# Kernel tuning notes

Hardware: AMD Instinct MI355X
Metric: run time of the kernel (lower is better)

The kernel has to match this reference:

```python
import jax, jax.numpy as jnp
import numpy as np

B, V = 256, 2048
PD, MD, H = 1024, 512, 512

def setup_inputs() -> dict:
    key = jax.random.key(0)
    k1, k2, k3, k4, k5 = jax.random.split(key, 5)
    patient_emb = jax.random.normal(k1, (B, PD), dtype=jnp.float32)
    atc4_emb = jax.random.normal(k2, (V, MD), dtype=jnp.float32)
    # Linear(PD+MD -> H): weight (H, PD+MD), bias (H,)
    W1 = jax.random.normal(k3, (H, PD + MD), dtype=jnp.float32) * 0.02
    b1 = jnp.zeros((H,), dtype=jnp.float32)
    # Linear(H -> 1): weight (1, H) -> store as (H,), bias scalar
    w2 = jax.random.normal(k4, (H,), dtype=jnp.float32) * 0.05
    b2 = jnp.zeros((), dtype=jnp.float32)
    return {"patient_emb": patient_emb, "atc4_emb": atc4_emb,
            "W1": W1, "b1": b1, "w2": w2, "b2": b2}

def reference(patient_emb, atc4_emb, W1, b1, w2, b2):
    # Algebraically equivalent to cat([patient, mol]) @ W1.T:
    # split W1 into patient and mol blocks, matmul each, broadcast-add.
    W1p = W1[:, :PD]   # (H, PD)
    W1m = W1[:, PD:]   # (H, MD)
    hp = jnp.einsum('bp,hp->bh', patient_emb, W1p)   # (B, H)
    hm = jnp.einsum('vm,hm->vh', atc4_emb, W1m)      # (V, H)
    h = jnp.tanh(hp[:, None, :] + hm[None, :, :] + b1)  # (B, V, H)
    scores = jnp.einsum('bvh,h->bv', h, w2) + b2     # (B, V)
    return scores
```

## Files before the change

### kernel.cpp

```cpp
#include <hip/hip_runtime.h>
#include <hip/hip_bf16.h>
#include <math.h>

typedef __attribute__((ext_vector_type(8))) short short8;
typedef __attribute__((ext_vector_type(4))) float float4v;
typedef __attribute__((ext_vector_type(2))) float float2v;

__device__ __forceinline__ float2v lo2(float4v v) {
    return __builtin_shufflevector(v, v, 0, 1);
}
__device__ __forceinline__ float2v hi2(float4v v) {
    return __builtin_shufflevector(v, v, 2, 3);
}

__device__ __forceinline__ int2 cvt2bf16x4(float4v v) {
    union { __hip_bfloat162 h2; int i; } u0, u1;
    u0.h2 = __float22bfloat162_rn(make_float2(v.x, v.y));
    u1.h2 = __float22bfloat162_rn(make_float2(v.z, v.w));
    return make_int2(u0.i, u1.i);
}

__global__ __launch_bounds__(256) void gemm_exp(
    const float* __restrict__ patient, const float* __restrict__ atc4,
    const float* __restrict__ W1, const float* __restrict__ b1,
    float* __restrict__ EA, float* __restrict__ EM)
{
    const float* A; const float* W; const float* bias; float* T;
    int lda, K, M;
    if (blockIdx.z == 0) {
        if (blockIdx.x >= 4) return;
        A = patient; lda = 1024; K = 1024; M = 256; bias = b1; T = EA; W = W1;
    } else {
        A = atc4;    lda = 512;  K = 512;  M = 2048; bias = nullptr; T = EM; W = W1 + 1024;
    }
    const int ldw = 1536;

    __shared__ short As[64][72];
    __shared__ short Bs[64][72];
    const int t = threadIdx.x;
    const int m0 = blockIdx.x * 64;
    const int n0 = blockIdx.y * 64;
    const int wave = t >> 6;
    const int lane = t & 63;
    const int wm = (wave & 1) * 32;
    const int wn = (wave >> 1) * 32;
    const int lrow = lane & 15;
    const int quad = lane >> 4;

    float4v acc[2][2];
    #pragma unroll
    for (int i = 0; i < 2; i++)
        #pragma unroll
        for (int j = 0; j < 2; j++)
            acc[i][j] = (float4v){0.f, 0.f, 0.f, 0.f};

    const int sr = t >> 2;
    const int sc = (t & 3) * 16;

    float4v av[4], wv[4];
    {
        const float* ap = A + (size_t)(m0 + sr) * lda + sc;
        const float* wp = W + (size_t)(n0 + sr) * ldw + sc;
        #pragma unroll
        for (int ii = 0; ii < 4; ii++) {
            av[ii] = *(const float4v*)(ap + ii * 4);
            wv[ii] = *(const float4v*)(wp + ii * 4);
        }
    }

    for (int k0 = 0; k0 < K; k0 += 64) {
        #pragma unroll
        for (int ii = 0; ii < 4; ii++) {
            *(int2*)&As[sr][sc + ii * 4] = cvt2bf16x4(av[ii]);
            *(int2*)&Bs[sr][sc + ii * 4] = cvt2bf16x4(wv[ii]);
        }
        __syncthreads();
        if (k0 + 64 < K) {
            const float* ap = A + (size_t)(m0 + sr) * lda + (k0 + 64 + sc);
            const float* wp = W + (size_t)(n0 + sr) * ldw + (k0 + 64 + sc);
            #pragma unroll
            for (int ii = 0; ii < 4; ii++) {
                av[ii] = *(const float4v*)(ap + ii * 4);
                wv[ii] = *(const float4v*)(wp + ii * 4);
            }
        }
        #pragma unroll
        for (int kk = 0; kk < 64; kk += 32) {
            short8 af[2], bfr[2];
            #pragma unroll
            for (int i = 0; i < 2; i++)
                af[i] = *(const short8*)&As[wm + i * 16 + lrow][kk + quad * 8];
            #pragma unroll
            for (int j = 0; j < 2; j++)
                bfr[j] = *(const short8*)&Bs[wn + j * 16 + lrow][kk + quad * 8];
            #pragma unroll
            for (int i = 0; i < 2; i++)
                #pragma unroll
                for (int j = 0; j < 2; j++)
                    acc[i][j] = __builtin_amdgcn_mfma_f32_16x16x32_bf16(
                        af[i], bfr[j], acc[i][j], 0, 0, 0);
        }
        __syncthreads();
    }

    #pragma unroll
    for (int i = 0; i < 2; i++) {
        #pragma unroll
        for (int j = 0; j < 2; j++) {
            const int n  = n0 + wn + j * 16 + lrow;
            const int mb = m0 + wm + i * 16 + quad * 4;
            const float bn = bias ? bias[n] : 0.0f;
            float4v ev;
            #pragma unroll
            for (int r = 0; r < 4; r++)
                ev[r] = __expf(2.0f * (acc[i][j][r] + bn));
            *(float4v*)&T[(size_t)n * M + mb] = ev;
        }
    }
}

__device__ __forceinline__ void rat4(
    float2v em0, float2v em1, float2v em2, float2v em3,
    float2v a0, float2v a1, float2v a2, float2v a3,
    float2v c0, float2v c1, float2v c2, float2v c3,
    float2v& acc)
{
    const float2v one2 = {1.f, 1.f};
    float2v d0 = __builtin_elementwise_fma(em0, a0, one2);
    float2v d1 = __builtin_elementwise_fma(em1, a1, one2);
    float2v d2 = __builtin_elementwise_fma(em2, a2, one2);
    float2v d3 = __builtin_elementwise_fma(em3, a3, one2);
    float2v e01 = d0 * d1;
    float2v e23 = d2 * d3;
    float2v n01 = __builtin_elementwise_fma(d1, c0, d0 * c1);
    float2v n23 = __builtin_elementwise_fma(d3, c2, d2 * c3);
    float2v num = __builtin_elementwise_fma(n01, e23, n23 * e01);
    float2v den = e01 * e23;
    float2v r = { __builtin_amdgcn_rcpf(den.x), __builtin_amdgcn_rcpf(den.y) };
    acc = __builtin_elementwise_fma(num, r, acc);
}

__global__ __launch_bounds__(256) void pair_kernel(
    const float* __restrict__ EA, const float* __restrict__ EM,
    const float* __restrict__ w2, float* __restrict__ partial)
{
    __shared__ float sEA[32][68];
    __shared__ float sEM[32][132];
    __shared__ float4v sC4[32];
    const int t  = threadIdx.x;
    const int v0 = blockIdx.x * 128;
    const int b0 = blockIdx.y * 64;
    const int h0 = blockIdx.z * 128;
    const int tx = t & 15;
    const int ty = t >> 4;

    if (t < 32) {
        float4v wvq = *(const float4v*)(w2 + h0 + 4 * t);
        sC4[t] = -2.0f * wvq;
    }

    float2v accAL[4], accAH[4], accBL[4], accBH[4];
    #pragma unroll
    for (int i = 0; i < 4; i++) {
        accAL[i] = (float2v){0.f, 0.f};  accAH[i] = (float2v){0.f, 0.f};
        accBL[i] = (float2v){0.f, 0.f};  accBH[i] = (float2v){0.f, 0.f};
    }

    const int rS = t >> 3;
    const int cA = (t & 7) * 8;
    const int cM = (t & 7) * 16;

    float4v pA0, pA1, pM0, pM1, pM2, pM3;
    {
        const float* pa = EA + (size_t)(h0 + rS) * 256 + b0 + cA;
        pA0 = *(const float4v*)pa;  pA1 = *(const float4v*)(pa + 4);
        const float* pm = EM + (size_t)(h0 + rS) * 2048 + v0 + cM;
        pM0 = *(const float4v*)pm;       pM1 = *(const float4v*)(pm + 4);
        pM2 = *(const float4v*)(pm + 8); pM3 = *(const float4v*)(pm + 12);
    }
    *(float4v*)&sEA[rS][cA] = pA0;      *(float4v*)&sEA[rS][cA + 4] = pA1;
    *(float4v*)&sEM[rS][cM] = pM0;      *(float4v*)&sEM[rS][cM + 4] = pM1;
    *(float4v*)&sEM[rS][cM + 8] = pM2;  *(float4v*)&sEM[rS][cM + 12] = pM3;
    __syncthreads();

    #pragma unroll 1
    for (int s = 0; s < 4; s++) {
        if (s < 3) {
            const int hr = h0 + (s + 1) * 32 + rS;
            const float* pa = EA + (size_t)hr * 256 + b0 + cA;
            pA0 = *(const float4v*)pa;  pA1 = *(const float4v*)(pa + 4);
            const float* pm = EM + (size_t)hr * 2048 + v0 + cM;
            pM0 = *(const float4v*)pm;       pM1 = *(const float4v*)(pm + 4);
            pM2 = *(const float4v*)(pm + 8); pM3 = *(const float4v*)(pm + 12);
        }
        #pragma unroll 2
        for (int q = 0; q < 8; q++) {
            const int hq = 4 * q;
            const float4v ea0 = *(const float4v*)&sEA[hq    ][ty * 4];
            const float4v ea1 = *(const float4v*)&sEA[hq + 1][ty * 4];
            const float4v ea2 = *(const float4v*)&sEA[hq + 2][ty * 4];
            const float4v ea3 = *(const float4v*)&sEA[hq + 3][ty * 4];
            const float4v c = sC4[s * 8 + q];
            const float2v c0 = { c.x, c.x };
            const float2v c1 = { c.y, c.y };
            const float2v c2 = { c.z, c.z };
            const float2v c3 = { c.w, c.w };
            {
                const float4v em0 = *(const float4v*)&sEM[hq    ][tx * 4];
                const float4v em1 = *(const float4v*)&sEM[hq + 1][tx * 4];
                const float4v em2 = *(const float4v*)&sEM[hq + 2][tx * 4];
                const float4v em3 = *(const float4v*)&sEM[hq + 3][tx * 4];
                const float2v em0L = lo2(em0), em0H = hi2(em0);
                const float2v em1L = lo2(em1), em1H = hi2(em1);
                const float2v em2L = lo2(em2), em2H = hi2(em2);
                const float2v em3L = lo2(em3), em3H = hi2(em3);
                #pragma unroll
                for (int i = 0; i < 4; i++) {
                    const float2v a0 = { ea0[i], ea0[i] };
                    const float2v a1 = { ea1[i], ea1[i] };
                    const float2v a2 = { ea2[i], ea2[i] };
                    const float2v a3 = { ea3[i], ea3[i] };
                    rat4(em0L, em1L, em2L, em3L, a0, a1, a2, a3,
                         c0, c1, c2, c3, accAL[i]);
                    rat4(em0H, em1H, em2H, em3H, a0, a1, a2, a3,
                         c0, c1, c2, c3, accAH[i]);
                }
            }
            {
                const float4v em0 = *(const float4v*)&sEM[hq    ][64 + tx * 4];
                const float4v em1 = *(const float4v*)&sEM[hq + 1][64 + tx * 4];
                const float4v em2 = *(const float4v*)&sEM[hq + 2][64 + tx * 4];
                const float4v em3 = *(const float4v*)&sEM[hq + 3][64 + tx * 4];
                const float2v em0L = lo2(em0), em0H = hi2(em0);
                const float2v em1L = lo2(em1), em1H = hi2(em1);
                const float2v em2L = lo2(em2), em2H = hi2(em2);
                const float2v em3L = lo2(em3), em3H = hi2(em3);
                #pragma unroll
                for (int i = 0; i < 4; i++) {
                    const float2v a0 = { ea0[i], ea0[i] };
                    const float2v a1 = { ea1[i], ea1[i] };
                    const float2v a2 = { ea2[i], ea2[i] };
                    const float2v a3 = { ea3[i], ea3[i] };
                    rat4(em0L, em1L, em2L, em3L, a0, a1, a2, a3,
                         c0, c1, c2, c3, accBL[i]);
                    rat4(em0H, em1H, em2H, em3H, a0, a1, a2, a3,
                         c0, c1, c2, c3, accBH[i]);
                }
            }
        }
        if (s < 3) {
            __syncthreads();
            *(float4v*)&sEA[rS][cA] = pA0;      *(float4v*)&sEA[rS][cA + 4] = pA1;
            *(float4v*)&sEM[rS][cM] = pM0;      *(float4v*)&sEM[rS][cM + 4] = pM1;
            *(float4v*)&sEM[rS][cM + 8] = pM2;  *(float4v*)&sEM[rS][cM + 12] = pM3;
            __syncthreads();
        }
    }

    float4v w2q = sC4[0];
    #pragma unroll
    for (int k = 1; k < 32; k++) w2q += sC4[k];
    const float w2s = -0.5f * (w2q.x + w2q.y + w2q.z + w2q.w);

    const size_t pb = (size_t)blockIdx.z * (256 * 2048);
    #pragma unroll
    for (int i = 0; i < 4; i++) {
        const size_t row = pb + (size_t)(b0 + ty * 4 + i) * 2048 + v0 + tx * 4;
        float4v oA = { accAL[i].x + w2s, accAL[i].y + w2s,
                       accAH[i].x + w2s, accAH[i].y + w2s };
        float4v oB = { accBL[i].x + w2s, accBL[i].y + w2s,
                       accBH[i].x + w2s, accBH[i].y + w2s };
        *(float4v*)&partial[row] = oA;
        *(float4v*)&partial[row + 64] = oB;
    }
}

__global__ __launch_bounds__(256) void reduce_kernel(
    const float* __restrict__ partial, const float* __restrict__ b2,
    float* __restrict__ out)
{
    const int i = (blockIdx.x * 256 + threadIdx.x) * 4;
    const float bb = b2[0];
    float4v s = *(const float4v*)&partial[i];
    #pragma unroll
    for (int z = 1; z < 4; z++)
        s += *(const float4v*)&partial[(size_t)z * 524288 + i];
    float4v o = s + bb;
    *(float4v*)&out[i] = o;
}

extern "C" void kernel_launch(void* const* d_in, const int* in_sizes, int n_in,
                              void* d_out, int out_size, void* d_ws, size_t ws_size,
                              hipStream_t stream)
{
    const float* patient = (const float*)d_in[0];
    const float* atc4    = (const float*)d_in[1];
    const float* W1      = (const float*)d_in[2];
    const float* b1      = (const float*)d_in[3];
    const float* w2      = (const float*)d_in[4];
    const float* b2      = (const float*)d_in[5];
    float* out = (float*)d_out;
    float* ws  = (float*)d_ws;

    float* EA      = ws;
    float* EM      = ws + 131072;
    float* partial = ws + 1179648;

    gemm_exp<<<dim3(32, 8, 2), 256, 0, stream>>>(patient, atc4, W1, b1, EA, EM);
    pair_kernel<<<dim3(16, 4, 4), 256, 0, stream>>>(EA, EM, w2, partial);
    reduce_kernel<<<512, 256, 0, stream>>>(partial, b2, out);
}
```

Measured before the change: 117.3 us.

## Double-buffer pair-kernel LDS tiles and fuse split-H reduction via last-block atomics

The shared-memory tiles in the pair kernel are double-buffered, and global loads are issued two stages ahead, so each stage needs one barrier instead of two. The separate reduce kernel is removed. Each output tile's last-finishing H-split block, found through an atomic counter zeroed by the GEMM kernel, sums the four partials and adds b2. This saves a kernel launch and overlaps the reduction with other blocks, at the cost of more LDS per block, thread fences, and a serialized tail in the final blocks.

```diff
diff --git a/kernel.cpp b/kernel.cpp
--- a/kernel.cpp
+++ b/kernel.cpp
@@ -23,8 +23,11 @@
 __global__ __launch_bounds__(256) void gemm_exp(
     const float* __restrict__ patient, const float* __restrict__ atc4,
     const float* __restrict__ W1, const float* __restrict__ b1,
-    float* __restrict__ EA, float* __restrict__ EM)
+    float* __restrict__ EA, float* __restrict__ EM, int* __restrict__ ctr)
 {
+    if (blockIdx.z == 0 && blockIdx.x == 0 && blockIdx.y == 0 && threadIdx.x < 64)
+        ctr[threadIdx.x] = 0;
+
     const float* A; const float* W; const float* bias; float* T;
     int lda, K, M;
     if (blockIdx.z == 0) {
@@ -142,11 +145,14 @@
 
 __global__ __launch_bounds__(256) void pair_kernel(
     const float* __restrict__ EA, const float* __restrict__ EM,
-    const float* __restrict__ w2, float* __restrict__ partial)
+    const float* __restrict__ w2, const float* __restrict__ b2,
+    float* __restrict__ partial, float* __restrict__ out,
+    int* __restrict__ ctr)
 {
-    __shared__ float sEA[32][68];
-    __shared__ float sEM[32][132];
+    __shared__ float sEA[2][32][68];
+    __shared__ float sEM[2][32][132];
     __shared__ float4v sC4[32];
+    __shared__ int isLast;
     const int t  = threadIdx.x;
     const int v0 = blockIdx.x * 128;
     const int b0 = blockIdx.y * 64;
@@ -178,15 +184,28 @@
         pM0 = *(const float4v*)pm;       pM1 = *(const float4v*)(pm + 4);
         pM2 = *(const float4v*)(pm + 8); pM3 = *(const float4v*)(pm + 12);
     }
-    *(float4v*)&sEA[rS][cA] = pA0;      *(float4v*)&sEA[rS][cA + 4] = pA1;
-    *(float4v*)&sEM[rS][cM] = pM0;      *(float4v*)&sEM[rS][cM + 4] = pM1;
-    *(float4v*)&sEM[rS][cM + 8] = pM2;  *(float4v*)&sEM[rS][cM + 12] = pM3;
+    *(float4v*)&sEA[0][rS][cA] = pA0;      *(float4v*)&sEA[0][rS][cA + 4] = pA1;
+    *(float4v*)&sEM[0][rS][cM] = pM0;      *(float4v*)&sEM[0][rS][cM + 4] = pM1;
+    *(float4v*)&sEM[0][rS][cM + 8] = pM2;  *(float4v*)&sEM[0][rS][cM + 12] = pM3;
+    {
+        const float* pa = EA + (size_t)(h0 + 32 + rS) * 256 + b0 + cA;
+        pA0 = *(const float4v*)pa;  pA1 = *(const float4v*)(pa + 4);
+        const float* pm = EM + (size_t)(h0 + 32 + rS) * 2048 + v0 + cM;
+        pM0 = *(const float4v*)pm;       pM1 = *(const float4v*)(pm + 4);
+        pM2 = *(const float4v*)(pm + 8); pM3 = *(const float4v*)(pm + 12);
+    }
     __syncthreads();
 
     #pragma unroll 1
     for (int s = 0; s < 4; s++) {
+        const int cur = s & 1, nxt = cur ^ 1;
         if (s < 3) {
-            const int hr = h0 + (s + 1) * 32 + rS;
+            *(float4v*)&sEA[nxt][rS][cA] = pA0;      *(float4v*)&sEA[nxt][rS][cA + 4] = pA1;
+            *(float4v*)&sEM[nxt][rS][cM] = pM0;      *(float4v*)&sEM[nxt][rS][cM + 4] = pM1;
+            *(float4v*)&sEM[nxt][rS][cM + 8] = pM2;  *(float4v*)&sEM[nxt][rS][cM + 12] = pM3;
+        }
+        if (s < 2) {
+            const int hr = h0 + (s + 2) * 32 + rS;
             const float* pa = EA + (size_t)hr * 256 + b0 + cA;
             pA0 = *(const float4v*)pa;  pA1 = *(const float4v*)(pa + 4);
             const float* pm = EM + (size_t)hr * 2048 + v0 + cM;
@@ -196,20 +215,20 @@
         #pragma unroll 2
         for (int q = 0; q < 8; q++) {
             const int hq = 4 * q;
-            const float4v ea0 = *(const float4v*)&sEA[hq    ][ty * 4];
-            const float4v ea1 = *(const float4v*)&sEA[hq + 1][ty * 4];
-            const float4v ea2 = *(const float4v*)&sEA[hq + 2][ty * 4];
-            const float4v ea3 = *(const float4v*)&sEA[hq + 3][ty * 4];
+            const float4v ea0 = *(const float4v*)&sEA[cur][hq    ][ty * 4];
+            const float4v ea1 = *(const float4v*)&sEA[cur][hq + 1][ty * 4];
+            const float4v ea2 = *(const float4v*)&sEA[cur][hq + 2][ty * 4];
+            const float4v ea3 = *(const float4v*)&sEA[cur][hq + 3][ty * 4];
             const float4v c = sC4[s * 8 + q];
             const float2v c0 = { c.x, c.x };
             const float2v c1 = { c.y, c.y };
             const float2v c2 = { c.z, c.z };
             const float2v c3 = { c.w, c.w };
             {
-                const float4v em0 = *(const float4v*)&sEM[hq    ][tx * 4];
-                const float4v em1 = *(const float4v*)&sEM[hq + 1][tx * 4];
-                const float4v em2 = *(const float4v*)&sEM[hq + 2][tx * 4];
-                const float4v em3 = *(const float4v*)&sEM[hq + 3][tx * 4];
+                const float4v em0 = *(const float4v*)&sEM[cur][hq    ][tx * 4];
+                const float4v em1 = *(const float4v*)&sEM[cur][hq + 1][tx * 4];
+                const float4v em2 = *(const float4v*)&sEM[cur][hq + 2][tx * 4];
+                const float4v em3 = *(const float4v*)&sEM[cur][hq + 3][tx * 4];
                 const float2v em0L = lo2(em0), em0H = hi2(em0);
                 const float2v em1L = lo2(em1), em1H = hi2(em1);
                 const float2v em2L = lo2(em2), em2H = hi2(em2);
@@ -227,10 +246,10 @@
                 }
             }
             {
-                const float4v em0 = *(const float4v*)&sEM[hq    ][64 + tx * 4];
-                const float4v em1 = *(const float4v*)&sEM[hq + 1][64 + tx * 4];
-                const float4v em2 = *(const float4v*)&sEM[hq + 2][64 + tx * 4];
-                const float4v em3 = *(const float4v*)&sEM[hq + 3][64 + tx * 4];
+                const float4v em0 = *(const float4v*)&sEM[cur][hq    ][64 + tx * 4];
+                const float4v em1 = *(const float4v*)&sEM[cur][hq + 1][64 + tx * 4];
+                const float4v em2 = *(const float4v*)&sEM[cur][hq + 2][64 + tx * 4];
+                const float4v em3 = *(const float4v*)&sEM[cur][hq + 3][64 + tx * 4];
                 const float2v em0L = lo2(em0), em0H = hi2(em0);
                 const float2v em1L = lo2(em1), em1H = hi2(em1);
                 const float2v em2L = lo2(em2), em2H = hi2(em2);
@@ -248,13 +267,7 @@
                 }
             }
         }
-        if (s < 3) {
-            __syncthreads();
-            *(float4v*)&sEA[rS][cA] = pA0;      *(float4v*)&sEA[rS][cA + 4] = pA1;
-            *(float4v*)&sEM[rS][cM] = pM0;      *(float4v*)&sEM[rS][cM + 4] = pM1;
-            *(float4v*)&sEM[rS][cM + 8] = pM2;  *(float4v*)&sEM[rS][cM + 12] = pM3;
-            __syncthreads();
-        }
+        __syncthreads();
     }
 
     float4v w2q = sC4[0];
@@ -273,20 +286,28 @@
         *(float4v*)&partial[row] = oA;
         *(float4v*)&partial[row + 64] = oB;
     }
-}
-
-__global__ __launch_bounds__(256) void reduce_kernel(
-    const float* __restrict__ partial, const float* __restrict__ b2,
-    float* __restrict__ out)
-{
-    const int i = (blockIdx.x * 256 + threadIdx.x) * 4;
-    const float bb = b2[0];
-    float4v s = *(const float4v*)&partial[i];
-    #pragma unroll
-    for (int z = 1; z < 4; z++)
-        s += *(const float4v*)&partial[(size_t)z * 524288 + i];
-    float4v o = s + bb;
-    *(float4v*)&out[i] = o;
+
+    __threadfence();
+    if (t == 0)
+        isLast = (atomicAdd(&ctr[blockIdx.x * 4 + blockIdx.y], 1) == 3);
+    __syncthreads();
+    if (isLast) {
+        __threadfence();
+        const float bb = b2[0];
+        #pragma unroll
+        for (int k = 0; k < 8; k++) {
+            const int f = k * 256 + t;
+            const int row = f >> 5;
+            const int col = (f & 31) << 2;
+            const float* p = partial + (size_t)(b0 + row) * 2048 + v0 + col;
+            float4v sum = *(const float4v*)p;
+            sum += *(const float4v*)(p + 524288);
+            sum += *(const float4v*)(p + 2 * 524288);
+            sum += *(const float4v*)(p + 3 * 524288);
+            float4v o = sum + bb;
+            *(float4v*)&out[(size_t)(b0 + row) * 2048 + v0 + col] = o;
+        }
+    }
 }
 
 extern "C" void kernel_launch(void* const* d_in, const int* in_sizes, int n_in,
@@ -305,8 +326,8 @@
     float* EA      = ws;
     float* EM      = ws + 131072;
     float* partial = ws + 1179648;
-
-    gemm_exp<<<dim3(32, 8, 2), 256, 0, stream>>>(patient, atc4, W1, b1, EA, EM);
-    pair_kernel<<<dim3(16, 4, 4), 256, 0, stream>>>(EA, EM, w2, partial);
-    reduce_kernel<<<512, 256, 0, stream>>>(partial, b2, out);
-}
+    int*   ctr     = (int*)(ws + 1179648 + 4 * 524288);
+
+    gemm_exp<<<dim3(32, 8, 2), 256, 0, stream>>>(patient, atc4, W1, b1, EA, EM, ctr);
+    pair_kernel<<<dim3(16, 4, 4), 256, 0, stream>>>(EA, EM, w2, b2, partial, out, ctr);
+}
```

Result: slower. 144.7 us (+23.3%).
